# Optimization experiments

Measured on AMD Instinct MI355X. Metric: run time of the kernel, lower is better.

Reference implementation:

```python
import jax, jax.numpy as jnp
import numpy as np

D_MODEL = 128
N_HEADS = 4
HEAD_DIM = D_MODEL // N_HEADS


def setup_inputs() -> dict:
    key = jax.random.key(0)
    ks = jax.random.split(key, 16)
    s = 0.05
    B, N, T = 1, 1024, 1024
    return {
        "node_states": jax.random.normal(ks[0], (B, N, D_MODEL), jnp.float32),
        "task_features": jax.random.normal(ks[1], (T, D_MODEL), jnp.float32),
        "in_proj_w": jax.random.normal(ks[2], (3 * D_MODEL, D_MODEL), jnp.float32) * s,
        "in_proj_b": jnp.zeros((3 * D_MODEL,), jnp.float32),
        "out_w": jax.random.normal(ks[3], (D_MODEL, D_MODEL), jnp.float32) * s,
        "out_b": jnp.zeros((D_MODEL,), jnp.float32),
        "W1": jax.random.normal(ks[4], (256, 256), jnp.float32) * s,
        "b1": jnp.zeros((256,), jnp.float32),
        "W2": jax.random.normal(ks[5], (128, 256), jnp.float32) * s,
        "b2": jnp.zeros((128,), jnp.float32),
        "W3": jax.random.normal(ks[6], (1, 128), jnp.float32) * s,
        "b3": jnp.zeros((1,), jnp.float32),
        "Wc1": jax.random.normal(ks[7], (256, D_MODEL), jnp.float32) * s,
        "bc1": jnp.zeros((256,), jnp.float32),
        "Wc2": jax.random.normal(ks[8], (32, 256), jnp.float32) * s,
        "bc2": jnp.zeros((32,), jnp.float32),
    }


def _mha(x, in_proj_w, in_proj_b, out_w, out_b):
    # x: [B, N, D]; torch nn.MultiheadAttention self-attention, batch_first.
    B, N, D = x.shape
    q = x @ in_proj_w[:D].T + in_proj_b[:D]
    k = x @ in_proj_w[D:2 * D].T + in_proj_b[D:2 * D]
    v = x @ in_proj_w[2 * D:].T + in_proj_b[2 * D:]
    def split(t):  # [B,N,D] -> [B,H,N,dh]
        return t.reshape(B, N, N_HEADS, HEAD_DIM).transpose(0, 2, 1, 3)
    qh, kh, vh = split(q), split(k), split(v)
    scores = jnp.einsum("bhqd,bhkd->bhqk", qh, kh) / jnp.sqrt(jnp.float32(HEAD_DIM))
    attn = jax.nn.softmax(scores, axis=-1)  # [B,H,N,N]
    ctx = jnp.einsum("bhqk,bhkd->bhqd", attn, vh)
    ctx = ctx.transpose(0, 2, 1, 3).reshape(B, N, D)
    out = ctx @ out_w.T + out_b
    attn_avg = attn.mean(axis=1)  # torch averages heads by default -> [B,N,N]
    return out, attn_avg


def reference(node_states, task_features, in_proj_w, in_proj_b, out_w, out_b,
              W1, b1, W2, b2, W3, b3, Wc1, bc1, Wc2, bc2):
    attended, attn_w = _mha(node_states, in_proj_w, in_proj_b, out_w, out_b)
    nodes = attended[0]  # original loop only uses batch 0: [N, D]
    # Linear on concat([task, node]) == split-weight sum; vectorize pairwise.
    t1 = task_features @ W1[:, :D_MODEL].T          # [T, 256]
    n1 = nodes @ W1[:, D_MODEL:].T                  # [N, 256]
    h1 = jax.nn.relu(t1[:, None, :] + n1[None, :, :] + b1)      # [T, N, 256]
    h2 = jax.nn.relu(jnp.einsum("tnc,kc->tnk", h1, W2) + b2)   # [T, N, 128]
    matching_scores = jax.nn.sigmoid(jnp.einsum("tnk,ok->tn", h2, W3) + b3[0])
    global_state = attended.mean(axis=1)            # [B, D]
    coordination_logits = jax.nn.relu(global_state @ Wc1.T + bc1) @ Wc2.T + bc2
    return matching_scores, coordination_logits, attn_w
```

## Files before the change

kernel.cpp:

```cpp
#include <hip/hip_runtime.h>
#include <hip/hip_fp16.h>
#include <stdint.h>


typedef __attribute__((ext_vector_type(4))) float floatx4;
typedef __attribute__((ext_vector_type(8))) _Float16 half8;

#define OFF_QKV  0x000000u
#define OFF_T1H  0x280000u
#define OFF_N1H  0x300000u
#define OFF_W2F  0x380000u
#define OFF_GS   0x398000u
#define OFF_SM   0x3A0000u
#define OFF_SL   0x3A8000u
#define OFF_SC   0x400000u
#define OFF_CTP  0xC00000u

__device__ __forceinline__ unsigned pkadd(unsigned a, unsigned b) {
    unsigned r; asm("v_pk_add_f16 %0, %1, %2" : "=v"(r) : "v"(a), "v"(b)); return r;
}
__device__ __forceinline__ unsigned pkmax(unsigned a, unsigned b) {
    unsigned r; asm("v_pk_max_f16 %0, %1, %2" : "=v"(r) : "v"(a), "v"(b)); return r;
}
__device__ __forceinline__ unsigned pk2h(float a, float b) {
    return (unsigned)__half_as_ushort(__float2half(a)) |
           ((unsigned)__half_as_ushort(__float2half(b)) << 16);
}
__device__ __forceinline__ float h2f(unsigned short u) {
    return __half2float(__ushort_as_half(u));
}

template<bool BIAS, bool F16OUT>
__device__ __forceinline__ void gemm_dev(
    const float* __restrict__ A, int lda,
    const float* __restrict__ B, int ldb,
    const float* __restrict__ bias,
    void* __restrict__ Cv, int ldc, int K, float scale,
    int m0, int n0, float (*As)[64], float (*Bs)[64])
{
    const int tid = threadIdx.x;
    const int tx = tid & 15, ty = tid >> 4;
    const int lr = tid >> 2;
    const int lk = (tid & 3) * 4;
    float c[4][4] = {};

    for (int k0 = 0; k0 < K; k0 += 16) {
        float4 a  = *(const float4*)&A[(long)(m0 + lr) * lda + k0 + lk];
        float4 bb = *(const float4*)&B[(long)(n0 + lr) * ldb + k0 + lk];
        __syncthreads();
        As[lk + 0][lr] = a.x;  As[lk + 1][lr] = a.y;  As[lk + 2][lr] = a.z;  As[lk + 3][lr] = a.w;
        Bs[lk + 0][lr] = bb.x; Bs[lk + 1][lr] = bb.y; Bs[lk + 2][lr] = bb.z; Bs[lk + 3][lr] = bb.w;
        __syncthreads();
#pragma unroll
        for (int k = 0; k < 16; k++) {
            float4 av = *(const float4*)&As[k][ty * 4];
            float4 bv = *(const float4*)&Bs[k][tx * 4];
            c[0][0] += av.x * bv.x; c[0][1] += av.x * bv.y; c[0][2] += av.x * bv.z; c[0][3] += av.x * bv.w;
            c[1][0] += av.y * bv.x; c[1][1] += av.y * bv.y; c[1][2] += av.y * bv.z; c[1][3] += av.y * bv.w;
            c[2][0] += av.z * bv.x; c[2][1] += av.z * bv.y; c[2][2] += av.z * bv.z; c[2][3] += av.z * bv.w;
            c[3][0] += av.w * bv.x; c[3][1] += av.w * bv.y; c[3][2] += av.w * bv.z; c[3][3] += av.w * bv.w;
        }
    }

    float bsv[4] = {0.f, 0.f, 0.f, 0.f};
    if (BIAS) {
        float4 t = *(const float4*)&bias[n0 + tx * 4];
        bsv[0] = t.x; bsv[1] = t.y; bsv[2] = t.z; bsv[3] = t.w;
    }
#pragma unroll
    for (int i = 0; i < 4; i++) {
        float v0 = c[i][0] * scale + bsv[0];
        float v1 = c[i][1] * scale + bsv[1];
        float v2 = c[i][2] * scale + bsv[2];
        float v3 = c[i][3] * scale + bsv[3];
        long m = m0 + ty * 4 + i;
        if (F16OUT) {
            unsigned short* Cp = (unsigned short*)Cv;
            ushort4 o;
            o.x = __half_as_ushort(__float2half(v0));
            o.y = __half_as_ushort(__float2half(v1));
            o.z = __half_as_ushort(__float2half(v2));
            o.w = __half_as_ushort(__float2half(v3));
            *(ushort4*)&Cp[m * ldc + n0 + tx * 4] = o;
        } else {
            float* Cp = (float*)Cv;
            *(float4*)&Cp[m * ldc + n0 + tx * 4] = make_float4(v0, v1, v2, v3);
        }
    }
}

__launch_bounds__(256)
__global__ void proj_fused(const float* __restrict__ node, const float* __restrict__ ipw,
                           const float* __restrict__ ipb,
                           const float* __restrict__ task, const float* __restrict__ W1,
                           const float* __restrict__ b1, const float* __restrict__ W2,
                           float* __restrict__ qkv, unsigned short* __restrict__ t1h,
                           unsigned short* __restrict__ w2f, float* __restrict__ gs)
{
    __shared__ float As[16][64], Bs[16][64];
    const int bid = blockIdx.x;
    if (bid < 96) {
        gemm_dev<true, false>(node, 128, ipw, 128, ipb, qkv, 384, 128, 1.0f,
                              (bid & 15) * 64, (bid >> 4) * 64, As, Bs);
    } else if (bid < 160) {
        const int b = bid - 96;
        gemm_dev<true, true>(task, 128, W1, 256, b1, t1h, 256, 128, 1.0f,
                             (b & 15) * 64, (b >> 4) * 64, As, Bs);
    } else if (bid < 176) {
        const int gtid = (bid - 160) * 256 + threadIdx.x;
        const int lane = gtid & 63, frag = gtid >> 6;
        const int cc = frag >> 3, ot = frag & 7;
        const float* src = &W2[(ot * 16 + (lane & 15)) * 256 + cc * 32 + (lane >> 4) * 8];
        uint4 o;
        o.x = pk2h(src[0], src[1]);
        o.y = pk2h(src[2], src[3]);
        o.z = pk2h(src[4], src[5]);
        o.w = pk2h(src[6], src[7]);
        ((uint4*)w2f)[gtid] = o;
    } else {
        if (threadIdx.x < 128) gs[threadIdx.x] = 0.f;
    }
}

__launch_bounds__(256)
__global__ void scores_kernel(const float* __restrict__ qkv, unsigned short* __restrict__ sc16)
{
    __shared__ float As[16][64], Bs[16][64];
    const int h = blockIdx.z;
    gemm_dev<false, true>(qkv + h * 32, 384, qkv + 128 + h * 32, 384, nullptr,
                          sc16 + ((size_t)h << 20), 1024, 32, 0.17677669529663687f,
                          blockIdx.x * 64, blockIdx.y * 64, As, Bs);
}

__launch_bounds__(256)
__global__ void attn_pre(const unsigned short* __restrict__ sc16,
                         float* __restrict__ sm, float* __restrict__ sl,
                         float* __restrict__ attn_out)
{
    __shared__ float Ps[4][1024];
    __shared__ float stm[4], stl[4];
    const int t = threadIdx.x;
    const int q = blockIdx.x;

#pragma unroll
    for (int h = 0; h < 4; h++) {
        ushort4 u = *(const ushort4*)&sc16[((size_t)h << 20) + (size_t)q * 1024 + t * 4];
        *(float4*)&Ps[h][t * 4] = make_float4(h2f(u.x), h2f(u.y), h2f(u.z), h2f(u.w));
    }
    __syncthreads();

    {
        const int h = t >> 6, ln = t & 63;
        float4 v[4];
        float mx = -1e30f;
#pragma unroll
        for (int i = 0; i < 4; i++) {
            v[i] = *(const float4*)&Ps[h][ln * 4 + i * 256];
            mx = fmaxf(mx, fmaxf(fmaxf(v[i].x, v[i].y), fmaxf(v[i].z, v[i].w)));
        }
#pragma unroll
        for (int m = 1; m < 64; m <<= 1) mx = fmaxf(mx, __shfl_xor(mx, m));
        float s = 0.f;
#pragma unroll
        for (int i = 0; i < 4; i++)
            s += __expf(v[i].x - mx) + __expf(v[i].y - mx) +
                 __expf(v[i].z - mx) + __expf(v[i].w - mx);
#pragma unroll
        for (int m = 1; m < 64; m <<= 1) s += __shfl_xor(s, m);
        if (ln == 0) {
            stm[h] = mx; stl[h] = s;
            sm[h * 1024 + q] = mx; sl[h * 1024 + q] = s;
        }
    }
    __syncthreads();

    float a0 = 0.f, a1 = 0.f, a2 = 0.f, a3 = 0.f;
#pragma unroll
    for (int h = 0; h < 4; h++) {
        const float m = stm[h], il = 1.0f / stl[h];
        float4 f = *(const float4*)&Ps[h][t * 4];
        a0 += __expf(f.x - m) * il;
        a1 += __expf(f.y - m) * il;
        a2 += __expf(f.z - m) * il;
        a3 += __expf(f.w - m) * il;
    }
    *(float4*)&attn_out[(size_t)q * 1024 + t * 4] =
        make_float4(0.25f * a0, 0.25f * a1, 0.25f * a2, 0.25f * a3);
}

__launch_bounds__(256)
__global__ void ctx_kernel(const unsigned short* __restrict__ sc16,
                           const float* __restrict__ sm, const float* __restrict__ sl,
                           const float* __restrict__ qkv, float* __restrict__ ctxp)
{
    const int h = blockIdx.z;
    const int q0 = blockIdx.x * 64;
    const int ks = blockIdx.y;
    const int kbase = ks * 128;
    __shared__ float As[32][64];
    __shared__ float Vs[32][32];
    const int tid = threadIdx.x;
    const int tx = tid & 15, ty = tid >> 4;
    const int sq = tid >> 3;
    const int sk4 = (tid & 7) * 4;
    float acc[4][2] = {};

    for (int k0 = kbase; k0 < kbase + 128; k0 += 32) {
        __syncthreads();
#pragma unroll
        for (int half = 0; half < 2; half++) {
            int q = sq + half * 32;
            float m = sm[h * 1024 + q0 + q];
            float il = 1.0f / sl[h * 1024 + q0 + q];
            ushort4 u = *(const ushort4*)&sc16[((size_t)h << 20) + (size_t)(q0 + q) * 1024 + k0 + sk4];
            As[sk4 + 0][q] = __expf(h2f(u.x) - m) * il;
            As[sk4 + 1][q] = __expf(h2f(u.y) - m) * il;
            As[sk4 + 2][q] = __expf(h2f(u.z) - m) * il;
            As[sk4 + 3][q] = __expf(h2f(u.w) - m) * il;
        }
        *(float4*)&Vs[sq][sk4] = *(const float4*)&qkv[(long)(k0 + sq) * 384 + 256 + h * 32 + sk4];
        __syncthreads();
#pragma unroll
        for (int k = 0; k < 32; k++) {
            float4 a = *(const float4*)&As[k][tx * 4];
            float b0 = Vs[k][ty * 2], b1 = Vs[k][ty * 2 + 1];
            acc[0][0] += a.x * b0; acc[0][1] += a.x * b1;
            acc[1][0] += a.y * b0; acc[1][1] += a.y * b1;
            acc[2][0] += a.z * b0; acc[2][1] += a.z * b1;
            acc[3][0] += a.w * b0; acc[3][1] += a.w * b1;
        }
    }
#pragma unroll
    for (int i = 0; i < 4; i++) {
        *(float2*)&ctxp[((size_t)ks * 1024 + (q0 + tx * 4 + i)) * 128 + h * 32 + ty * 2] =
            make_float2(acc[i][0], acc[i][1]);
    }
}

__launch_bounds__(256)
__global__ void attn_post(const float* __restrict__ ctxp, const float* __restrict__ outw,
                          const float* __restrict__ outb, const float* __restrict__ W1,
                          unsigned short* __restrict__ n1h, float* __restrict__ gs)
{
    __shared__ float ctxs[4][128];
    __shared__ float attr[4][128];
    const int t = threadIdx.x;
    const int q0 = blockIdx.x * 4;

#pragma unroll
    for (int s = 0; s < 2; s++) {
        const int idx = s * 256 + t;
        const int q = idx >> 7, d = idx & 127;
        float v = 0.f;
#pragma unroll
        for (int ks = 0; ks < 8; ks++)
            v += ctxp[((size_t)ks * 1024 + (q0 + q)) * 128 + d];
        ctxs[q][d] = v;
    }
    __syncthreads();

    {
        const int j = t & 127, qp = t >> 7;
        float a0 = outb[j], a1 = a0;
        const float* wr = &outw[j * 128];
        for (int d = 0; d < 128; d += 4) {
            float4 w  = *(const float4*)&wr[d];
            float4 c0 = *(const float4*)&ctxs[qp * 2 + 0][d];
            float4 c1 = *(const float4*)&ctxs[qp * 2 + 1][d];
            a0 += w.x * c0.x + w.y * c0.y + w.z * c0.z + w.w * c0.w;
            a1 += w.x * c1.x + w.y * c1.y + w.z * c1.z + w.w * c1.w;
        }
        attr[qp * 2 + 0][j] = a0;
        attr[qp * 2 + 1][j] = a1;
    }
    __syncthreads();
    if (t < 128) atomicAdd(&gs[t], attr[0][t] + attr[1][t] + attr[2][t] + attr[3][t]);

    {
        const int c = t;
        const float* wr = &W1[c * 256 + 128];
        float n[4] = {};
        for (int d = 0; d < 128; d += 4) {
            float4 w = *(const float4*)&wr[d];
#pragma unroll
            for (int q = 0; q < 4; q++) {
                float4 a = *(const float4*)&attr[q][d];
                n[q] += w.x * a.x + w.y * a.y + w.z * a.z + w.w * a.w;
            }
        }
#pragma unroll
        for (int q = 0; q < 4; q++)
            n1h[(size_t)(q0 + q) * 256 + c] = __half_as_ushort(__float2half(n[q]));
    }
}

__launch_bounds__(256, 2)
__global__ void score_kernel(const unsigned short* __restrict__ t1h,
                             const unsigned short* __restrict__ n1h,
                             const unsigned short* __restrict__ w2f,
                             const float* __restrict__ b2, const float* __restrict__ W3,
                             const float* __restrict__ b3, float* __restrict__ out,
                             const float* __restrict__ gs,
                             const float* __restrict__ Wc1, const float* __restrict__ bc1,
                             const float* __restrict__ Wc2, const float* __restrict__ bc2,
                             float* __restrict__ outc)
{
    __shared__ unsigned short w2s[32768];
    __shared__ float b2s[128], w3s[128];
    const int tid = threadIdx.x;

    if (blockIdx.y == 32) {
        if (blockIdx.x != 0) return;
        float* g  = (float*)w2s;
        float* hh = g + 128;
        if (tid < 128) g[tid] = gs[tid] * (1.0f / 1024.0f);
        __syncthreads();
        {
            float a = bc1[tid];
            const float* wr = &Wc1[tid * 128];
            for (int d = 0; d < 128; d += 4) {
                float4 w = *(const float4*)&wr[d];
                a += w.x * g[d] + w.y * g[d + 1] + w.z * g[d + 2] + w.w * g[d + 3];
            }
            hh[tid] = fmaxf(a, 0.f);
        }
        __syncthreads();
        if (tid < 32) {
            float a = bc2[tid];
            const float* wr = &Wc2[tid * 256];
            for (int c = 0; c < 256; c += 4) {
                float4 w = *(const float4*)&wr[c];
                a += w.x * hh[c] + w.y * hh[c + 1] + w.z * hh[c + 2] + w.w * hh[c + 3];
            }
            outc[tid] = a;
        }
        return;
    }

    const int lane = tid & 63;
    const int wv = tid >> 6;
    const int col = lane & 15;
    const int quad = lane >> 4;
    const int nb = blockIdx.x * 64 + wv * 16;
    const int tb = blockIdx.y * 32;

    {
        const uint4* src = (const uint4*)w2f;
        uint4* dst = (uint4*)w2s;
#pragma unroll
        for (int i = 0; i < 16; i++) dst[tid + i * 256] = src[tid + i * 256];
        if (tid < 128) { b2s[tid] = b2[tid]; w3s[tid] = W3[tid]; }
    }

    const unsigned short* nbase = n1h + (size_t)(nb + col) * 256 + quad * 8;
    const unsigned short* tbase = t1h + (size_t)tb * 256 + quad * 8;
    const float b3s = b3[0];
    __syncthreads();

    uint4 np_c = *(const uint4*)(nbase);
    uint4 tp_c[4];
#pragma unroll
    for (int tt = 0; tt < 4; tt++)
        tp_c[tt] = *(const uint4*)(tbase + (size_t)tt * 256);

    for (int tg = 0; tg < 8; tg++) {
        floatx4 acc[4][8];
#pragma unroll
        for (int ot = 0; ot < 8; ot++) {
            float4 bq = *(const float4*)&b2s[ot * 16 + quad * 4];
            floatx4 bi = {bq.x, bq.y, bq.z, bq.w};
#pragma unroll
            for (int tt = 0; tt < 4; tt++) acc[tt][ot] = bi;
        }

#pragma unroll
        for (int cc = 0; cc < 8; cc++) {
            const int ncc = (cc + 1) & 7;
            const int ntg = (cc == 7) ? ((tg + 1) & 7) : tg;
            uint4 np_n = *(const uint4*)(nbase + ncc * 32);
            uint4 tp_n[4];
#pragma unroll
            for (int tt = 0; tt < 4; tt++)
                tp_n[tt] = *(const uint4*)(tbase + (size_t)(ntg * 4 + tt) * 256 + ncc * 32);

            const unsigned* npu = (const unsigned*)&np_c;
            union { unsigned u[4]; half8 h; } af[4];
#pragma unroll
            for (int tt = 0; tt < 4; tt++) {
                const unsigned* tpu = (const unsigned*)&tp_c[tt];
#pragma unroll
                for (int p = 0; p < 4; p++)
                    af[tt].u[p] = pkmax(pkadd(tpu[p], npu[p]), 0u);
            }
            __builtin_amdgcn_s_setprio(1);
#pragma unroll
            for (int ot = 0; ot < 8; ot++) {
                union { uint4 u; half8 h; } bf;
                bf.u = *(const uint4*)&w2s[((cc * 8 + ot) * 64 + lane) * 8];
#pragma unroll
                for (int tt = 0; tt < 4; tt++)
                    acc[tt][ot] = __builtin_amdgcn_mfma_f32_16x16x32_f16(bf.h, af[tt].h, acc[tt][ot], 0, 0, 0);
            }
            __builtin_amdgcn_s_setprio(0);

            np_c = np_n;
#pragma unroll
            for (int tt = 0; tt < 4; tt++) tp_c[tt] = tp_n[tt];
        }

        float part[4] = {0.f, 0.f, 0.f, 0.f};
#pragma unroll
        for (int ot = 0; ot < 8; ot++) {
            float4 wq = *(const float4*)&w3s[ot * 16 + quad * 4];
#pragma unroll
            for (int tt = 0; tt < 4; tt++) {
                floatx4 a = acc[tt][ot];
                part[tt] += fmaxf(a[0], 0.f) * wq.x + fmaxf(a[1], 0.f) * wq.y
                          + fmaxf(a[2], 0.f) * wq.z + fmaxf(a[3], 0.f) * wq.w;
            }
        }
        float outv = 0.f;
#pragma unroll
        for (int tt = 0; tt < 4; tt++) {
            float p = part[tt];
            p += __shfl_xor(p, 16);
            p += __shfl_xor(p, 32);
            if (quad == tt) outv = p;
        }
        out[(size_t)(tb + tg * 4 + quad) * 1024 + nb + col] =
            1.0f / (1.0f + __expf(-(outv + b3s)));
    }
}

extern "C" void kernel_launch(void* const* d_in, const int* in_sizes, int n_in,
                              void* d_out, int out_size, void* d_ws, size_t ws_size,
                              hipStream_t stream)
{
    const float* node = (const float*)d_in[0];
    const float* task = (const float*)d_in[1];
    const float* ipw  = (const float*)d_in[2];
    const float* ipb  = (const float*)d_in[3];
    const float* outw = (const float*)d_in[4];
    const float* outb = (const float*)d_in[5];
    const float* W1   = (const float*)d_in[6];
    const float* b1   = (const float*)d_in[7];
    const float* W2   = (const float*)d_in[8];
    const float* b2   = (const float*)d_in[9];
    const float* W3   = (const float*)d_in[10];
    const float* b3   = (const float*)d_in[11];
    const float* Wc1  = (const float*)d_in[12];
    const float* bc1  = (const float*)d_in[13];
    const float* Wc2  = (const float*)d_in[14];
    const float* bc2  = (const float*)d_in[15];

    char* ws = (char*)d_ws;
    float* qkv = (float*)(ws + OFF_QKV);
    unsigned short* t1h = (unsigned short*)(ws + OFF_T1H);
    unsigned short* n1h = (unsigned short*)(ws + OFF_N1H);
    unsigned short* w2f = (unsigned short*)(ws + OFF_W2F);
    float* gs = (float*)(ws + OFF_GS);
    float* sm = (float*)(ws + OFF_SM);
    float* sl = (float*)(ws + OFF_SL);
    unsigned short* sc16 = (unsigned short*)(ws + OFF_SC);
    float* ctxp = (float*)(ws + OFF_CTP);

    float* out_match = (float*)d_out;
    float* out_coord = out_match + 1048576;
    float* out_attn  = out_coord + 32;

    proj_fused<<<dim3(177, 1, 1), 256, 0, stream>>>(
        node, ipw, ipb, task, W1, b1, W2, qkv, t1h, w2f, gs);
    scores_kernel<<<dim3(16, 16, 4), 256, 0, stream>>>(qkv, sc16);
    attn_pre<<<dim3(1024, 1, 1), 256, 0, stream>>>(sc16, sm, sl, out_attn);
    ctx_kernel<<<dim3(16, 8, 4), 256, 0, stream>>>(sc16, sm, sl, qkv, ctxp);
    attn_post<<<dim3(256, 1, 1), 256, 0, stream>>>(ctxp, outw, outb, W1, n1h, gs);
    score_kernel<<<dim3(16, 33, 1), 256, 0, stream>>>(
        t1h, n1h, w2f, b2, W3, b3, out_match,
        gs, Wc1, bc1, Wc2, bc2, out_coord);
}
```

Before: 196.3 us.

## Move attention score and context GEMMs to fp16 MFMA with packed Q/K/V

The QKV projection now also writes fp16 copies of Q and K plus a transposed V. The scores and context kernels are rewritten to use 16x16x32 fp16 MFMA instructions instead of scalar-FMA shared-memory GEMMs. attn_pre now writes normalized fp16 probabilities in place over the score buffer, so the context kernel no longer recomputes exp and no longer needs the softmax max/sum buffers. This cuts scalar arithmetic and exp recomputation, at the cost of fp16 rounding of the probabilities and scattered 2-byte transposed stores for V.

```diff
diff --git a/kernel.cpp b/kernel.cpp
--- a/kernel.cpp
+++ b/kernel.cpp
@@ -7,12 +7,13 @@
 typedef __attribute__((ext_vector_type(8))) _Float16 half8;
 
 #define OFF_QKV  0x000000u
+#define OFF_Q16  0x180000u
+#define OFF_K16  0x1C0000u
+#define OFF_V16  0x200000u
 #define OFF_T1H  0x280000u
 #define OFF_N1H  0x300000u
 #define OFF_W2F  0x380000u
 #define OFF_GS   0x398000u
-#define OFF_SM   0x3A0000u
-#define OFF_SL   0x3A8000u
 #define OFF_SC   0x400000u
 #define OFF_CTP  0xC00000u
 
@@ -29,14 +30,20 @@
 __device__ __forceinline__ float h2f(unsigned short u) {
     return __half2float(__ushort_as_half(u));
 }
-
-template<bool BIAS, bool F16OUT>
+__device__ __forceinline__ unsigned short f2h(float v) {
+    return __half_as_ushort(__float2half(v));
+}
+
+template<bool BIAS, bool F16OUT, bool SIDE>
 __device__ __forceinline__ void gemm_dev(
     const float* __restrict__ A, int lda,
     const float* __restrict__ B, int ldb,
     const float* __restrict__ bias,
     void* __restrict__ Cv, int ldc, int K, float scale,
-    int m0, int n0, float (*As)[64], float (*Bs)[64])
+    int m0, int n0, float (*As)[64], float (*Bs)[64],
+    unsigned short* __restrict__ q16o,
+    unsigned short* __restrict__ k16o,
+    unsigned short* __restrict__ v16o)
 {
     const int tid = threadIdx.x;
     const int tx = tid & 15, ty = tid >> 4;
@@ -67,6 +74,7 @@
         float4 t = *(const float4*)&bias[n0 + tx * 4];
         bsv[0] = t.x; bsv[1] = t.y; bsv[2] = t.z; bsv[3] = t.w;
     }
+    const int gcol = n0 + tx * 4;
 #pragma unroll
     for (int i = 0; i < 4; i++) {
         float v0 = c[i][0] * scale + bsv[0];
@@ -77,14 +85,25 @@
         if (F16OUT) {
             unsigned short* Cp = (unsigned short*)Cv;
             ushort4 o;
-            o.x = __half_as_ushort(__float2half(v0));
-            o.y = __half_as_ushort(__float2half(v1));
-            o.z = __half_as_ushort(__float2half(v2));
-            o.w = __half_as_ushort(__float2half(v3));
+            o.x = f2h(v0); o.y = f2h(v1); o.z = f2h(v2); o.w = f2h(v3);
             *(ushort4*)&Cp[m * ldc + n0 + tx * 4] = o;
         } else {
             float* Cp = (float*)Cv;
             *(float4*)&Cp[m * ldc + n0 + tx * 4] = make_float4(v0, v1, v2, v3);
+        }
+        if (SIDE) {
+            ushort4 o;
+            o.x = f2h(v0); o.y = f2h(v1); o.z = f2h(v2); o.w = f2h(v3);
+            if (gcol < 128) {
+                *(ushort4*)&q16o[m * 128 + gcol] = o;
+            } else if (gcol < 256) {
+                *(ushort4*)&k16o[m * 128 + (gcol - 128)] = o;
+            } else {
+                v16o[(size_t)(gcol - 256 + 0) * 1024 + m] = o.x;
+                v16o[(size_t)(gcol - 256 + 1) * 1024 + m] = o.y;
+                v16o[(size_t)(gcol - 256 + 2) * 1024 + m] = o.z;
+                v16o[(size_t)(gcol - 256 + 3) * 1024 + m] = o.w;
+            }
         }
     }
 }
@@ -95,17 +114,22 @@
                            const float* __restrict__ task, const float* __restrict__ W1,
                            const float* __restrict__ b1, const float* __restrict__ W2,
                            float* __restrict__ qkv, unsigned short* __restrict__ t1h,
-                           unsigned short* __restrict__ w2f, float* __restrict__ gs)
+                           unsigned short* __restrict__ w2f, float* __restrict__ gs,
+                           unsigned short* __restrict__ q16,
+                           unsigned short* __restrict__ k16,
+                           unsigned short* __restrict__ v16t)
 {
     __shared__ float As[16][64], Bs[16][64];
     const int bid = blockIdx.x;
     if (bid < 96) {
-        gemm_dev<true, false>(node, 128, ipw, 128, ipb, qkv, 384, 128, 1.0f,
-                              (bid & 15) * 64, (bid >> 4) * 64, As, Bs);
+        gemm_dev<true, false, true>(node, 128, ipw, 128, ipb, qkv, 384, 128, 1.0f,
+                                    (bid & 15) * 64, (bid >> 4) * 64, As, Bs,
+                                    q16, k16, v16t);
     } else if (bid < 160) {
         const int b = bid - 96;
-        gemm_dev<true, true>(task, 128, W1, 256, b1, t1h, 256, 128, 1.0f,
-                             (b & 15) * 64, (b >> 4) * 64, As, Bs);
+        gemm_dev<true, true, false>(task, 128, W1, 256, b1, t1h, 256, 128, 1.0f,
+                                    (b & 15) * 64, (b >> 4) * 64, As, Bs,
+                                    nullptr, nullptr, nullptr);
     } else if (bid < 176) {
         const int gtid = (bid - 160) * 256 + threadIdx.x;
         const int lane = gtid & 63, frag = gtid >> 6;
@@ -123,18 +147,38 @@
 }
 
 __launch_bounds__(256)
-__global__ void scores_kernel(const float* __restrict__ qkv, unsigned short* __restrict__ sc16)
-{
-    __shared__ float As[16][64], Bs[16][64];
+__global__ void scores_mfma(const unsigned short* __restrict__ q16,
+                            const unsigned short* __restrict__ k16,
+                            unsigned short* __restrict__ sc16)
+{
     const int h = blockIdx.z;
-    gemm_dev<false, true>(qkv + h * 32, 384, qkv + 128 + h * 32, 384, nullptr,
-                          sc16 + ((size_t)h << 20), 1024, 32, 0.17677669529663687f,
-                          blockIdx.x * 64, blockIdx.y * 64, As, Bs);
+    const int tid = threadIdx.x;
+    const int lane = tid & 63, wv = tid >> 6;
+    const int col = lane & 15, quad = lane >> 4;
+    const int q0 = blockIdx.x * 64 + wv * 16;
+    const int kb = blockIdx.y * 64;
+    unsigned short* dst = sc16 + ((size_t)h << 20);
+
+    union { uint4 u; half8 h8; } bf;
+    bf.u = *(const uint4*)&q16[(size_t)(q0 + col) * 128 + h * 32 + quad * 8];
+#pragma unroll
+    for (int kt = 0; kt < 4; kt++) {
+        union { uint4 u; half8 h8; } af;
+        af.u = *(const uint4*)&k16[(size_t)(kb + kt * 16 + col) * 128 + h * 32 + quad * 8];
+        floatx4 c = {0.f, 0.f, 0.f, 0.f};
+        c = __builtin_amdgcn_mfma_f32_16x16x32_f16(af.h8, bf.h8, c, 0, 0, 0);
+        ushort4 o;
+        o.x = f2h(c[0] * 0.17677669529663687f);
+        o.y = f2h(c[1] * 0.17677669529663687f);
+        o.z = f2h(c[2] * 0.17677669529663687f);
+        o.w = f2h(c[3] * 0.17677669529663687f);
+        *(ushort4*)&dst[(size_t)(q0 + col) * 1024 + kb + kt * 16 + quad * 4] = o;
+    }
 }
 
 __launch_bounds__(256)
 __global__ void attn_pre(const unsigned short* __restrict__ sc16,
-                         float* __restrict__ sm, float* __restrict__ sl,
+                         unsigned short* __restrict__ pb,
                          float* __restrict__ attn_out)
 {
     __shared__ float Ps[4][1024];
@@ -167,10 +211,7 @@
                  __expf(v[i].z - mx) + __expf(v[i].w - mx);
 #pragma unroll
         for (int m = 1; m < 64; m <<= 1) s += __shfl_xor(s, m);
-        if (ln == 0) {
-            stm[h] = mx; stl[h] = s;
-            sm[h * 1024 + q] = mx; sl[h * 1024 + q] = s;
-        }
+        if (ln == 0) { stm[h] = mx; stl[h] = s; }
     }
     __syncthreads();
 
@@ -179,61 +220,49 @@
     for (int h = 0; h < 4; h++) {
         const float m = stm[h], il = 1.0f / stl[h];
         float4 f = *(const float4*)&Ps[h][t * 4];
-        a0 += __expf(f.x - m) * il;
-        a1 += __expf(f.y - m) * il;
-        a2 += __expf(f.z - m) * il;
-        a3 += __expf(f.w - m) * il;
+        float p0 = __expf(f.x - m) * il;
+        float p1 = __expf(f.y - m) * il;
+        float p2 = __expf(f.z - m) * il;
+        float p3 = __expf(f.w - m) * il;
+        a0 += p0; a1 += p1; a2 += p2; a3 += p3;
+        ushort4 pw;
+        pw.x = f2h(p0); pw.y = f2h(p1); pw.z = f2h(p2); pw.w = f2h(p3);
+        *(ushort4*)&pb[((size_t)h << 20) + (size_t)q * 1024 + t * 4] = pw;
     }
     *(float4*)&attn_out[(size_t)q * 1024 + t * 4] =
         make_float4(0.25f * a0, 0.25f * a1, 0.25f * a2, 0.25f * a3);
 }
 
 __launch_bounds__(256)
-__global__ void ctx_kernel(const unsigned short* __restrict__ sc16,
-                           const float* __restrict__ sm, const float* __restrict__ sl,
-                           const float* __restrict__ qkv, float* __restrict__ ctxp)
+__global__ void ctx_mfma(const unsigned short* __restrict__ pb,
+                         const unsigned short* __restrict__ v16t,
+                         float* __restrict__ ctxp)
 {
     const int h = blockIdx.z;
+    const int ks = blockIdx.y;
     const int q0 = blockIdx.x * 64;
-    const int ks = blockIdx.y;
-    const int kbase = ks * 128;
-    __shared__ float As[32][64];
-    __shared__ float Vs[32][32];
     const int tid = threadIdx.x;
-    const int tx = tid & 15, ty = tid >> 4;
-    const int sq = tid >> 3;
-    const int sk4 = (tid & 7) * 4;
-    float acc[4][2] = {};
-
-    for (int k0 = kbase; k0 < kbase + 128; k0 += 32) {
-        __syncthreads();
-#pragma unroll
-        for (int half = 0; half < 2; half++) {
-            int q = sq + half * 32;
-            float m = sm[h * 1024 + q0 + q];
-            float il = 1.0f / sl[h * 1024 + q0 + q];
-            ushort4 u = *(const ushort4*)&sc16[((size_t)h << 20) + (size_t)(q0 + q) * 1024 + k0 + sk4];
-            As[sk4 + 0][q] = __expf(h2f(u.x) - m) * il;
-            As[sk4 + 1][q] = __expf(h2f(u.y) - m) * il;
-            As[sk4 + 2][q] = __expf(h2f(u.z) - m) * il;
-            As[sk4 + 3][q] = __expf(h2f(u.w) - m) * il;
-        }
-        *(float4*)&Vs[sq][sk4] = *(const float4*)&qkv[(long)(k0 + sq) * 384 + 256 + h * 32 + sk4];
-        __syncthreads();
-#pragma unroll
-        for (int k = 0; k < 32; k++) {
-            float4 a = *(const float4*)&As[k][tx * 4];
-            float b0 = Vs[k][ty * 2], b1 = Vs[k][ty * 2 + 1];
-            acc[0][0] += a.x * b0; acc[0][1] += a.x * b1;
-            acc[1][0] += a.y * b0; acc[1][1] += a.y * b1;
-            acc[2][0] += a.z * b0; acc[2][1] += a.z * b1;
-            acc[3][0] += a.w * b0; acc[3][1] += a.w * b1;
-        }
-    }
-#pragma unroll
-    for (int i = 0; i < 4; i++) {
-        *(float2*)&ctxp[((size_t)ks * 1024 + (q0 + tx * 4 + i)) * 128 + h * 32 + ty * 2] =
-            make_float2(acc[i][0], acc[i][1]);
+    const int lane = tid & 63, wv = tid >> 6;
+    const int col = lane & 15, quad = lane >> 4;
+    const unsigned short* ph = pb + ((size_t)h << 20);
+
+    floatx4 acc[2] = {};
+#pragma unroll
+    for (int kst = 0; kst < 4; kst++) {
+        const int k0 = ks * 128 + kst * 32;
+        union { uint4 u; half8 h8; } pf;
+        pf.u = *(const uint4*)&ph[(size_t)(q0 + wv * 16 + col) * 1024 + k0 + quad * 8];
+#pragma unroll
+        for (int dt = 0; dt < 2; dt++) {
+            union { uint4 u; half8 h8; } vf;
+            vf.u = *(const uint4*)&v16t[(size_t)(h * 32 + dt * 16 + col) * 1024 + k0 + quad * 8];
+            acc[dt] = __builtin_amdgcn_mfma_f32_16x16x32_f16(vf.h8, pf.h8, acc[dt], 0, 0, 0);
+        }
+    }
+#pragma unroll
+    for (int dt = 0; dt < 2; dt++) {
+        *(float4*)&ctxp[((size_t)ks * 1024 + q0 + wv * 16 + col) * 128 + h * 32 + dt * 16 + quad * 4] =
+            make_float4(acc[dt][0], acc[dt][1], acc[dt][2], acc[dt][3]);
     }
 }
 
@@ -455,12 +484,13 @@
 
     char* ws = (char*)d_ws;
     float* qkv = (float*)(ws + OFF_QKV);
+    unsigned short* q16 = (unsigned short*)(ws + OFF_Q16);
+    unsigned short* k16 = (unsigned short*)(ws + OFF_K16);
+    unsigned short* v16t = (unsigned short*)(ws + OFF_V16);
     unsigned short* t1h = (unsigned short*)(ws + OFF_T1H);
     unsigned short* n1h = (unsigned short*)(ws + OFF_N1H);
     unsigned short* w2f = (unsigned short*)(ws + OFF_W2F);
     float* gs = (float*)(ws + OFF_GS);
-    float* sm = (float*)(ws + OFF_SM);
-    float* sl = (float*)(ws + OFF_SL);
     unsigned short* sc16 = (unsigned short*)(ws + OFF_SC);
     float* ctxp = (float*)(ws + OFF_CTP);
 
@@ -469,10 +499,10 @@
     float* out_attn  = out_coord + 32;
 
     proj_fused<<<dim3(177, 1, 1), 256, 0, stream>>>(
-        node, ipw, ipb, task, W1, b1, W2, qkv, t1h, w2f, gs);
-    scores_kernel<<<dim3(16, 16, 4), 256, 0, stream>>>(qkv, sc16);
-    attn_pre<<<dim3(1024, 1, 1), 256, 0, stream>>>(sc16, sm, sl, out_attn);
-    ctx_kernel<<<dim3(16, 8, 4), 256, 0, stream>>>(sc16, sm, sl, qkv, ctxp);
+        node, ipw, ipb, task, W1, b1, W2, qkv, t1h, w2f, gs, q16, k16, v16t);
+    scores_mfma<<<dim3(16, 16, 4), 256, 0, stream>>>(q16, k16, sc16);
+    attn_pre<<<dim3(1024, 1, 1), 256, 0, stream>>>(sc16, sc16, out_attn);
+    ctx_mfma<<<dim3(16, 8, 4), 256, 0, stream>>>(sc16, v16t, ctxp);
     attn_post<<<dim3(256, 1, 1), 256, 0, stream>>>(ctxp, outw, outb, W1, n1h, gs);
     score_kernel<<<dim3(16, 33, 1), 256, 0, stream>>>(
         t1h, n1h, w2f, b2, W3, b3, out_match,
```

Result: no change. 193.9 us (-1.2%).
